# Performance work log

Measured on AMD Instinct MI355X. Metric: run time of the kernel, lower is better.

The kernel has to match this reference:

```python
import jax, jax.numpy as jnp
import numpy as np

B, L, D = 16, 1024, 768

def setup_inputs() -> dict:
    key = jax.random.key(0)
    ks = jax.random.split(key, 6)
    s = 1.0 / np.sqrt(D)  # torch Linear default init scale
    return {
        "h": jax.random.normal(ks[0], (B, L, D), dtype=jnp.float32),
        "q": jax.random.normal(ks[1], (B, L, D), dtype=jnp.float32),
        "w1_w": jax.random.uniform(ks[2], (L, D), jnp.float32, -s, s),
        "w1_b": jax.random.uniform(ks[3], (L,), jnp.float32, -s, s),
        "w2_w": jax.random.uniform(ks[4], (L, D), jnp.float32, -s, s),
        "w2_b": jax.random.uniform(ks[5], (L,), jnp.float32, -s, s),
    }

def reference(h, q, w1_w, w1_b, w2_w, w2_b):
    # w1h: [B, L, l], w2q: [B, L, l] -> permuted [B, l, L]
    w1h = jnp.einsum('bsd,ld->bsl', h, w1_w) + w1_b
    w2q = jnp.einsum('btd,ld->btl', q, w2_w) + w2_b
    w3hq = jnp.einsum('bsd,btd->bst', h, q)           # [B, L, L]
    a = w1h + jnp.swapaxes(w2q, 1, 2) + w3hq          # [B, L, L]
    p = jax.nn.softmax(a, axis=2)
    c = jnp.einsum('bst,btd->bsd', p, q)              # [B, L, D]
    m = jnp.max(a, axis=2)                            # [B, L]
    p2 = jax.nn.softmax(m, axis=1)                    # [B, L]
    qc = h * p2[:, :, None]                           # [B, L, D]
    return jnp.concatenate([h, c, h * c, qc * c], axis=2)  # [B, L, 4D]
```

## Files before the change

kernel.cpp:

```cpp
#include <hip/hip_runtime.h>
#include <stdint.h>

#define B_  16
#define L_  1024
#define D_  768
#define K1_ 1536

typedef unsigned short u16;
typedef __attribute__((ext_vector_type(4))) float f32x4;
typedef __attribute__((ext_vector_type(8))) _Float16 f16x8;

__device__ __forceinline__ u16 f2h(float x){
    return __builtin_bit_cast(u16, (_Float16)x);
}
__device__ __forceinline__ float h2f(u16 x){
    return (float)__builtin_bit_cast(_Float16, x);
}

__device__ __forceinline__ void gload_lds16(const void* g, void* l){
    __builtin_amdgcn_global_load_lds((const __attribute__((address_space(1))) void*)g,
                                     (__attribute__((address_space(3))) void*)l, 16, 0, 0);
}

__global__ __launch_bounds__(256) void prep(const float* __restrict__ h, const float* __restrict__ q,
    const float* __restrict__ w1w, const float* __restrict__ w2w,
    u16* __restrict__ hH, u16* __restrict__ wH, u16* __restrict__ qH,
    u16* __restrict__ w1h, u16* __restrict__ qT, int b0, int nb)
{
    __shared__ float tile[32][33];
    int bb = blockIdx.z, bg = b0 + bb;
    int t0 = blockIdx.x * 32, d0 = blockIdx.y * 32;
    int tid = threadIdx.x;
    int r  = tid >> 3;
    int c4 = (tid & 7) * 4;
    int t = t0 + r, d = d0 + c4;
    size_t goff = (size_t)t * D_ + d;

    float4 qv  = *(const float4*)(q   + (size_t)bg * L_ * D_ + goff);
    float4 hv  = *(const float4*)(h   + (size_t)bg * L_ * D_ + goff);
    float4 w2v = *(const float4*)(w2w + goff);

    tile[r][c4 + 0] = qv.x; tile[r][c4 + 1] = qv.y;
    tile[r][c4 + 2] = qv.z; tile[r][c4 + 3] = qv.w;

    size_t o = ((size_t)bb * L_ + t) * D_ + d;
    ushort4 a;
    a.x = f2h(hv.x); a.y = f2h(hv.y); a.z = f2h(hv.z); a.w = f2h(hv.w);
    *(ushort4*)(hH + o) = a;
    a.x = f2h(hv.x + w2v.x); a.y = f2h(hv.y + w2v.y);
    a.z = f2h(hv.z + w2v.z); a.w = f2h(hv.w + w2v.w);
    *(ushort4*)(wH + o) = a;
    a.x = f2h(qv.x); a.y = f2h(qv.y); a.z = f2h(qv.z); a.w = f2h(qv.w);
    *(ushort4*)(qH + o) = a;
    if (bb == 0){
        float4 w1v = *(const float4*)(w1w + goff);
        a.x = f2h(w1v.x); a.y = f2h(w1v.y); a.z = f2h(w1v.z); a.w = f2h(w1v.w);
        *(ushort4*)(w1h + goff) = a;
    }
    __syncthreads();
    int dr = tid >> 3;
    int tc = (tid & 7) * 4;
    ushort4 b;
    b.x = f2h(tile[tc + 0][dr]); b.y = f2h(tile[tc + 1][dr]);
    b.z = f2h(tile[tc + 2][dr]); b.w = f2h(tile[tc + 3][dr]);
    *(ushort4*)(qT + (size_t)bb * D_ * L_ + (size_t)(d0 + dr) * L_ + t0 + tc) = b;
}

__global__ __launch_bounds__(512) void gemm1(
    const u16* __restrict__ hH, const u16* __restrict__ wH,
    const u16* __restrict__ qH, const u16* __restrict__ w1h,
    const float* __restrict__ w1b, const float* __restrict__ w2b,
    u16* __restrict__ pT, float* __restrict__ mT, float* __restrict__ sT)
{
    __shared__ u16 ldsA[2][256 * 64];
    __shared__ u16 ldsB[2][256 * 64];
    int nwg = gridDim.x;
    int o = blockIdx.x;
    int wg = (o & 7) * (nwg >> 3) + (o >> 3);
    int bb = wg >> 4;
    int tl = wg & 15;
    int smb = tl >> 2, tnb = tl & 3;
    int s0 = smb * 256, t0 = tnb * 256;
    int tid = threadIdx.x;
    int lane = tid & 63, wid = tid >> 6;
    int wm2 = wid >> 2, wn2 = wid & 3;
    int l15 = lane & 15, l4 = lane >> 4;

    const u16* hHb = hH + (size_t)bb * L_ * D_;
    const u16* wHb = wH + (size_t)bb * L_ * D_;
    const u16* qHb = qH + (size_t)bb * L_ * D_;

    f32x4 acc[8][4];
    #pragma unroll
    for (int m = 0; m < 8; m++)
        #pragma unroll
        for (int n = 0; n < 4; n++)
            acc[m][n] = (f32x4){0.f, 0.f, 0.f, 0.f};

    auto stage = [&](int t){
        int kb = t * 64;
        bool inH = (kb < D_);
        const u16* As = inH ? hHb : wHb;
        const u16* Bs = inH ? w1h : qHb;
        int koff = inH ? kb : (kb - D_);
        int buf = t & 1;
        #pragma unroll
        for (int q = 0; q < 4; q++){
            int idx = q * 512 + tid;
            int row = idx >> 3, c = idx & 7;
            int cc = c ^ (row & 7);
            int dst = (q * 512 + wid * 64) * 8;
            gload_lds16(As + (size_t)(s0 + row) * D_ + koff + cc * 8, &ldsA[buf][dst]);
            gload_lds16(Bs + (size_t)(t0 + row) * D_ + koff + cc * 8, &ldsB[buf][dst]);
        }
    };

    stage(0);
    asm volatile("s_waitcnt vmcnt(0)" ::: "memory");
    __builtin_amdgcn_s_barrier();

    for (int t = 0; t < 24; t++){
        if (t + 1 < 24) stage(t + 1);
        int bsel = t & 1;
        #pragma unroll
        for (int kk = 0; kk < 2; kk++){
            f16x8 bf[4];
            #pragma unroll
            for (int n = 0; n < 4; n++){
                int row = wn2 * 64 + n * 16 + l15;
                int c = kk * 4 + l4;
                bf[n] = *(const f16x8*)&ldsB[bsel][(row * 8 + (c ^ (row & 7))) * 8];
            }
            #pragma unroll
            for (int mh = 0; mh < 2; mh++){
                f16x8 af[4];
                #pragma unroll
                for (int mi = 0; mi < 4; mi++){
                    int row = wm2 * 128 + (mh * 4 + mi) * 16 + l15;
                    int c = kk * 4 + l4;
                    af[mi] = *(const f16x8*)&ldsA[bsel][(row * 8 + (c ^ (row & 7))) * 8];
                }
                __builtin_amdgcn_s_setprio(1);
                #pragma unroll
                for (int mi = 0; mi < 4; mi++)
                    #pragma unroll
                    for (int n = 0; n < 4; n++)
                        acc[mh * 4 + mi][n] = __builtin_amdgcn_mfma_f32_16x16x32_f16(
                            af[mi], bf[n], acc[mh * 4 + mi][n], 0, 0, 0);
                __builtin_amdgcn_s_setprio(0);
            }
        }
        asm volatile("s_waitcnt vmcnt(0)" ::: "memory");
        __builtin_amdgcn_s_barrier();
    }

    u16* pRow = pT + (size_t)bb * L_ * L_;
    #pragma unroll
    for (int m = 0; m < 8; m++){
        #pragma unroll
        for (int r = 0; r < 4; r++){
            int s = s0 + wm2 * 128 + m * 16 + l4 * 4 + r;
            float w2v = w2b[s];
            float v[4];
            float tmax = -1e30f;
            #pragma unroll
            for (int n = 0; n < 4; n++){
                int tcol = t0 + wn2 * 64 + n * 16 + l15;
                v[n] = acc[m][n][r] + w1b[tcol] + w2v;
                tmax = fmaxf(tmax, v[n]);
            }
            #pragma unroll
            for (int o2 = 1; o2 < 16; o2 <<= 1)
                tmax = fmaxf(tmax, __shfl_xor(tmax, o2));
            float e[4];
            float gsum = 0.f;
            #pragma unroll
            for (int n = 0; n < 4; n++){
                e[n] = __expf(v[n] - tmax);
                gsum += e[n];
            }
            #pragma unroll
            for (int n = 0; n < 4; n++){
                int tcol = t0 + wn2 * 64 + n * 16 + l15;
                pRow[(size_t)s * L_ + tcol] = f2h(e[n]);
            }
            #pragma unroll
            for (int o2 = 1; o2 < 16; o2 <<= 1)
                gsum += __shfl_xor(gsum, o2);
            if (l15 == 0){
                size_t mo = ((size_t)bb * L_ + s) * 16 + tnb * 4 + wn2;
                mT[mo] = tmax;
                sT[mo] = gsum;
            }
        }
    }
}

__global__ __launch_bounds__(1024) void p2k(const float* __restrict__ mT, const float* __restrict__ sT,
                                            float* __restrict__ p2, float* __restrict__ sc, int b0)
{
    __shared__ float red[16];
    int bb = blockIdx.x, bg = b0 + bb;
    int tid = threadIdx.x;
    const float4* mv = (const float4*)(mT + ((size_t)bb * L_ + tid) * 16);
    float4 m0 = mv[0], m1 = mv[1], m2 = mv[2], m3 = mv[3];
    float mj[16] = {m0.x, m0.y, m0.z, m0.w, m1.x, m1.y, m1.z, m1.w,
                    m2.x, m2.y, m2.z, m2.w, m3.x, m3.y, m3.z, m3.w};
    float v = mj[0];
    #pragma unroll
    for (int i = 1; i < 16; i++) v = fmaxf(v, mj[i]);

    float mx = v;
    #pragma unroll
    for (int o = 32; o; o >>= 1) mx = fmaxf(mx, __shfl_xor(mx, o));
    if ((tid & 63) == 0) red[tid >> 6] = mx;
    __syncthreads();
    float m2g = red[0];
    #pragma unroll
    for (int i = 1; i < 16; i++) m2g = fmaxf(m2g, red[i]);
    float e = __expf(v - m2g);
    float sum = e;
    #pragma unroll
    for (int o = 32; o; o >>= 1) sum += __shfl_xor(sum, o);
    __syncthreads();
    if ((tid & 63) == 0) red[tid >> 6] = sum;
    __syncthreads();
    float st = 0.f;
    #pragma unroll
    for (int i = 0; i < 16; i++) st += red[i];
    p2[(size_t)bg * L_ + tid] = e / st;

    const float4* sv = (const float4*)(sT + ((size_t)bb * L_ + tid) * 16);
    float4 s0v = sv[0], s1v = sv[1], s2v = sv[2], s3v = sv[3];
    float sj[16] = {s0v.x, s0v.y, s0v.z, s0v.w, s1v.x, s1v.y, s1v.z, s1v.w,
                    s2v.x, s2v.y, s2v.z, s2v.w, s3v.x, s3v.y, s3v.z, s3v.w};
    float ej[16];
    float S = 0.f;
    #pragma unroll
    for (int j = 0; j < 16; j++){
        ej[j] = __expf(mj[j] - v);
        S += sj[j] * ej[j];
    }
    float invS = 1.0f / S;
    float* scb = sc + (size_t)bb * 16 * L_;
    #pragma unroll
    for (int j = 0; j < 16; j++)
        scb[j * L_ + tid] = ej[j] * invS;
}

__global__ __launch_bounds__(512) void gemm2(const u16* __restrict__ pT, const u16* __restrict__ qT,
    const float* __restrict__ sc, float* __restrict__ out, int b0)
{
    __shared__ u16 ldsA[2][256 * 64];
    __shared__ u16 ldsB[2][192 * 64];
    int nwg = gridDim.x;
    int o = blockIdx.x;
    int wg = ((nwg & 7) == 0) ? ((o & 7) * (nwg >> 3) + (o >> 3)) : o;
    int bb = wg >> 4;
    int tl = wg & 15;
    int smb = tl >> 2, dnb = tl & 3;
    int s0 = smb * 256, d0 = dnb * 192;
    int tid = threadIdx.x;
    int lane = tid & 63, wid = tid >> 6;
    int wm2 = wid >> 2, wn2 = wid & 3;
    int l15 = lane & 15, l4 = lane >> 4;

    const u16* Ab = pT + (size_t)bb * L_ * L_;
    const u16* Bb = qT + (size_t)bb * D_ * L_;
    const float* scb = sc + (size_t)bb * 16 * L_;

    f32x4 acc[8][3];
    #pragma unroll
    for (int m = 0; m < 8; m++)
        #pragma unroll
        for (int n = 0; n < 3; n++)
            acc[m][n] = (f32x4){0.f, 0.f, 0.f, 0.f};

    auto stage = [&](int t){
        int kb = t * 64;
        int buf = t & 1;
        #pragma unroll
        for (int qq = 0; qq < 4; qq++){
            int idx = qq * 512 + tid;
            int row = idx >> 3, c = idx & 7;
            int cc = c ^ (row & 7);
            gload_lds16(Ab + (size_t)(s0 + row) * L_ + kb + cc * 8,
                        &ldsA[buf][(qq * 512 + wid * 64) * 8]);
        }
        #pragma unroll
        for (int qq = 0; qq < 3; qq++){
            int idx = qq * 512 + tid;
            int row = idx >> 3, c = idx & 7;
            int cc = c ^ (row & 7);
            gload_lds16(Bb + (size_t)(d0 + row) * L_ + kb + cc * 8,
                        &ldsB[buf][(qq * 512 + wid * 64) * 8]);
        }
    };

    stage(0);
    asm volatile("s_waitcnt vmcnt(0)" ::: "memory");
    __builtin_amdgcn_s_barrier();

    for (int t = 0; t < 16; t++){
        if (t + 1 < 16) stage(t + 1);
        int bsel = t & 1;
        _Float16 sch[8];
        #pragma unroll
        for (int m = 0; m < 8; m++)
            sch[m] = (_Float16)scb[(size_t)t * L_ + s0 + wm2 * 128 + m * 16 + l15];
        #pragma unroll
        for (int kk = 0; kk < 2; kk++){
            f16x8 bf[3];
            #pragma unroll
            for (int n = 0; n < 3; n++){
                int row = wn2 * 48 + n * 16 + l15;
                int c = kk * 4 + l4;
                bf[n] = *(const f16x8*)&ldsB[bsel][(row * 8 + (c ^ (row & 7))) * 8];
            }
            #pragma unroll
            for (int mh = 0; mh < 2; mh++){
                f16x8 af[4];
                #pragma unroll
                for (int mi = 0; mi < 4; mi++){
                    int row = wm2 * 128 + (mh * 4 + mi) * 16 + l15;
                    int c = kk * 4 + l4;
                    af[mi] = *(const f16x8*)&ldsA[bsel][(row * 8 + (c ^ (row & 7))) * 8];
                    af[mi] = af[mi] * sch[mh * 4 + mi];
                }
                __builtin_amdgcn_s_setprio(1);
                #pragma unroll
                for (int mi = 0; mi < 4; mi++)
                    #pragma unroll
                    for (int n = 0; n < 3; n++)
                        acc[mh * 4 + mi][n] = __builtin_amdgcn_mfma_f32_16x16x32_f16(
                            af[mi], bf[n], acc[mh * 4 + mi][n], 0, 0, 0);
                __builtin_amdgcn_s_setprio(0);
            }
        }
        asm volatile("s_waitcnt vmcnt(0)" ::: "memory");
        __builtin_amdgcn_s_barrier();
    }

    float* oC = out + ((size_t)(b0 + bb) * L_) * (4 * D_) + D_;
    #pragma unroll
    for (int m = 0; m < 8; m++){
        int sbase = s0 + wm2 * 128 + m * 16 + l4 * 4;
        #pragma unroll
        for (int r = 0; r < 4; r++){
            int s = sbase + r;
            #pragma unroll
            for (int n = 0; n < 3; n++){
                int d = d0 + wn2 * 48 + n * 16 + l15;
                oC[(size_t)s * (4 * D_) + d] = acc[m][n][r];
            }
        }
    }
}

__global__ __launch_bounds__(192) void epi(const u16* __restrict__ hH,
    const float* __restrict__ p2, float* __restrict__ out, int b0)
{
    int rowid = blockIdx.x;
    int bb = rowid >> 10, s = rowid & 1023;
    int bg = b0 + bb;
    float p2v = p2[(size_t)bg * L_ + s];
    const u16* hR = hH + ((size_t)bb * L_ + s) * D_;
    float* oR = out + ((size_t)bg * L_ + s) * (4 * D_);
    int d = threadIdx.x * 4;
    float4 cv = *(const float4*)(oR + D_ + d);
    ushort4 hu = *(const ushort4*)(hR + d);
    float4 hv = {h2f(hu.x), h2f(hu.y), h2f(hu.z), h2f(hu.w)};
    float4 hc = {hv.x * cv.x, hv.y * cv.y, hv.z * cv.z, hv.w * cv.w};
    float4 qc = {p2v * hc.x, p2v * hc.y, p2v * hc.z, p2v * hc.w};
    *(float4*)(oR + d)          = hv;
    *(float4*)(oR + 2 * D_ + d) = hc;
    *(float4*)(oR + 3 * D_ + d) = qc;
}

extern "C" void kernel_launch(void* const* d_in, const int* in_sizes, int n_in,
                              void* d_out, int out_size, void* d_ws, size_t ws_size,
                              hipStream_t stream)
{
    const float* h   = (const float*)d_in[0];
    const float* q   = (const float*)d_in[1];
    const float* w1w = (const float*)d_in[2];
    const float* w1b = (const float*)d_in[3];
    const float* w2w = (const float*)d_in[4];
    const float* w2b = (const float*)d_in[5];
    float* out = (float*)d_out;

    const size_t szPlane = (size_t)L_ * D_ * 2;
    const size_t szM     = (size_t)B_ * L_ * 4;
    const size_t perB_pT = (size_t)L_ * L_ * 2;
    const size_t perB_s  = (size_t)L_ * 16 * 4;
    const size_t perB = 4 * szPlane + perB_pT + 3 * perB_s;
    const size_t fixed = szPlane + szM;

    int NB = 1;
    if (ws_size > fixed){
        size_t nbc = (ws_size - fixed) / perB;
        NB = (nbc >= 16) ? 16 : (nbc < 1 ? 1 : (int)nbc);
    }

    char* p = (char*)d_ws;
    u16*   w1h  = (u16*)p;   p += szPlane;
    float* p2   = (float*)p; p += szM;
    float* mT   = (float*)p; p += perB_s * NB;
    float* sT   = (float*)p; p += perB_s * NB;
    float* sc   = (float*)p; p += perB_s * NB;
    u16*   hH   = (u16*)p;   p += szPlane * NB;
    u16*   wH   = (u16*)p;   p += szPlane * NB;
    u16*   qH   = (u16*)p;   p += szPlane * NB;
    u16*   qT   = (u16*)p;   p += szPlane * NB;
    u16*   pT   = (u16*)p;

    for (int b0 = 0; b0 < B_; b0 += NB){
        int nb = (B_ - b0 < NB) ? (B_ - b0) : NB;
        prep  <<<dim3(32, 24, nb), 256, 0, stream>>>(h, q, w1w, w2w, hH, wH, qH, w1h, qT, b0, nb);
        gemm1 <<<dim3(16 * nb), 512, 0, stream>>>(hH, wH, qH, w1h, w1b, w2b, pT, mT, sT);
        p2k   <<<dim3(nb), 1024, 0, stream>>>(mT, sT, p2, sc, b0);
        gemm2 <<<dim3(16 * nb), 512, 0, stream>>>(pT, qT, sc, out, b0);
        epi   <<<dim3(nb * 1024), 192, 0, stream>>>(hH, p2, out, b0);
    }
}
```

Measured before the change: 193.9 us.

## Factor score GEMM as (h+w2)(w1+q) minus precomputed w2·w1 to halve K

The fused score GEMM used to concatenate two K=768 products ([h, h+w2]·[w1, q]). It now computes one K=768 product of (h+w2) and (w1+q), then subtracts a batch-independent w2·w1 term. That term is computed once by a new small GEMM kernel into an fp32 workspace and read back in the softmax epilogue. This halves the MFMA work and the operand loads in the main GEMM. In exchange it adds a one-time 16-block GEMM, extra fp32 reads of C0 per tile, more workspace, and possible fp16 rounding and cancellation error from the summed operands.

```diff
diff --git a/kernel.cpp b/kernel.cpp
--- a/kernel.cpp
+++ b/kernel.cpp
@@ -4,7 +4,6 @@
 #define B_  16
 #define L_  1024
 #define D_  768
-#define K1_ 1536
 
 typedef unsigned short u16;
 typedef __attribute__((ext_vector_type(4))) float f32x4;
@@ -24,8 +23,8 @@
 
 __global__ __launch_bounds__(256) void prep(const float* __restrict__ h, const float* __restrict__ q,
     const float* __restrict__ w1w, const float* __restrict__ w2w,
-    u16* __restrict__ hH, u16* __restrict__ wH, u16* __restrict__ qH,
-    u16* __restrict__ w1h, u16* __restrict__ qT, int b0, int nb)
+    u16* __restrict__ hH, u16* __restrict__ wH, u16* __restrict__ B1,
+    u16* __restrict__ w1h, u16* __restrict__ w2h, u16* __restrict__ qT, int b0, int nb)
 {
     __shared__ float tile[32][33];
     int bb = blockIdx.z, bg = b0 + bb;
@@ -39,6 +38,7 @@
     float4 qv  = *(const float4*)(q   + (size_t)bg * L_ * D_ + goff);
     float4 hv  = *(const float4*)(h   + (size_t)bg * L_ * D_ + goff);
     float4 w2v = *(const float4*)(w2w + goff);
+    float4 w1v = *(const float4*)(w1w + goff);
 
     tile[r][c4 + 0] = qv.x; tile[r][c4 + 1] = qv.y;
     tile[r][c4 + 2] = qv.z; tile[r][c4 + 3] = qv.w;
@@ -50,12 +50,14 @@
     a.x = f2h(hv.x + w2v.x); a.y = f2h(hv.y + w2v.y);
     a.z = f2h(hv.z + w2v.z); a.w = f2h(hv.w + w2v.w);
     *(ushort4*)(wH + o) = a;
-    a.x = f2h(qv.x); a.y = f2h(qv.y); a.z = f2h(qv.z); a.w = f2h(qv.w);
-    *(ushort4*)(qH + o) = a;
+    a.x = f2h(w1v.x + qv.x); a.y = f2h(w1v.y + qv.y);
+    a.z = f2h(w1v.z + qv.z); a.w = f2h(w1v.w + qv.w);
+    *(ushort4*)(B1 + o) = a;
     if (bb == 0){
-        float4 w1v = *(const float4*)(w1w + goff);
         a.x = f2h(w1v.x); a.y = f2h(w1v.y); a.z = f2h(w1v.z); a.w = f2h(w1v.w);
         *(ushort4*)(w1h + goff) = a;
+        a.x = f2h(w2v.x); a.y = f2h(w2v.y); a.z = f2h(w2v.z); a.w = f2h(w2v.w);
+        *(ushort4*)(w2h + goff) = a;
     }
     __syncthreads();
     int dr = tid >> 3;
@@ -66,10 +68,96 @@
     *(ushort4*)(qT + (size_t)bb * D_ * L_ + (size_t)(d0 + dr) * L_ + t0 + tc) = b;
 }
 
+__global__ __launch_bounds__(512) void c0k(const u16* __restrict__ w2h, const u16* __restrict__ w1h,
+                                           float* __restrict__ C0)
+{
+    __shared__ u16 ldsA[2][256 * 64];
+    __shared__ u16 ldsB[2][256 * 64];
+    int tl = blockIdx.x;
+    int smb = tl >> 2, tnb = tl & 3;
+    int s0 = smb * 256, t0 = tnb * 256;
+    int tid = threadIdx.x;
+    int lane = tid & 63, wid = tid >> 6;
+    int wm2 = wid >> 2, wn2 = wid & 3;
+    int l15 = lane & 15, l4 = lane >> 4;
+
+    f32x4 acc[8][4];
+    #pragma unroll
+    for (int m = 0; m < 8; m++)
+        #pragma unroll
+        for (int n = 0; n < 4; n++)
+            acc[m][n] = (f32x4){0.f, 0.f, 0.f, 0.f};
+
+    auto stage = [&](int t){
+        int kb = t * 64;
+        int buf = t & 1;
+        #pragma unroll
+        for (int q = 0; q < 4; q++){
+            int idx = q * 512 + tid;
+            int row = idx >> 3, c = idx & 7;
+            int cc = c ^ (row & 7);
+            int dst = (q * 512 + wid * 64) * 8;
+            gload_lds16(w2h + (size_t)(s0 + row) * D_ + kb + cc * 8, &ldsA[buf][dst]);
+            gload_lds16(w1h + (size_t)(t0 + row) * D_ + kb + cc * 8, &ldsB[buf][dst]);
+        }
+    };
+
+    stage(0);
+    asm volatile("s_waitcnt vmcnt(0)" ::: "memory");
+    __builtin_amdgcn_s_barrier();
+
+    for (int t = 0; t < 12; t++){
+        if (t + 1 < 12) stage(t + 1);
+        int bsel = t & 1;
+        #pragma unroll
+        for (int kk = 0; kk < 2; kk++){
+            f16x8 bf[4];
+            #pragma unroll
+            for (int n = 0; n < 4; n++){
+                int row = wn2 * 64 + n * 16 + l15;
+                int c = kk * 4 + l4;
+                bf[n] = *(const f16x8*)&ldsB[bsel][(row * 8 + (c ^ (row & 7))) * 8];
+            }
+            #pragma unroll
+            for (int mh = 0; mh < 2; mh++){
+                f16x8 af[4];
+                #pragma unroll
+                for (int mi = 0; mi < 4; mi++){
+                    int row = wm2 * 128 + (mh * 4 + mi) * 16 + l15;
+                    int c = kk * 4 + l4;
+                    af[mi] = *(const f16x8*)&ldsA[bsel][(row * 8 + (c ^ (row & 7))) * 8];
+                }
+                #pragma unroll
+                for (int mi = 0; mi < 4; mi++)
+                    #pragma unroll
+                    for (int n = 0; n < 4; n++)
+                        acc[mh * 4 + mi][n] = __builtin_amdgcn_mfma_f32_16x16x32_f16(
+                            af[mi], bf[n], acc[mh * 4 + mi][n], 0, 0, 0);
+            }
+        }
+        asm volatile("s_waitcnt vmcnt(0)" ::: "memory");
+        __builtin_amdgcn_s_barrier();
+    }
+
+    #pragma unroll
+    for (int m = 0; m < 8; m++){
+        int sbase = s0 + wm2 * 128 + m * 16 + l4 * 4;
+        #pragma unroll
+        for (int r = 0; r < 4; r++){
+            int s = sbase + r;
+            #pragma unroll
+            for (int n = 0; n < 4; n++){
+                int tcol = t0 + wn2 * 64 + n * 16 + l15;
+                C0[(size_t)s * L_ + tcol] = acc[m][n][r];
+            }
+        }
+    }
+}
+
 __global__ __launch_bounds__(512) void gemm1(
-    const u16* __restrict__ hH, const u16* __restrict__ wH,
-    const u16* __restrict__ qH, const u16* __restrict__ w1h,
+    const u16* __restrict__ wH, const u16* __restrict__ B1,
     const float* __restrict__ w1b, const float* __restrict__ w2b,
+    const float* __restrict__ C0,
     u16* __restrict__ pT, float* __restrict__ mT, float* __restrict__ sT)
 {
     __shared__ u16 ldsA[2][256 * 64];
@@ -86,9 +174,8 @@
     int wm2 = wid >> 2, wn2 = wid & 3;
     int l15 = lane & 15, l4 = lane >> 4;
 
-    const u16* hHb = hH + (size_t)bb * L_ * D_;
-    const u16* wHb = wH + (size_t)bb * L_ * D_;
-    const u16* qHb = qH + (size_t)bb * L_ * D_;
+    const u16* Ab = wH + (size_t)bb * L_ * D_;
+    const u16* Bb = B1 + (size_t)bb * L_ * D_;
 
     f32x4 acc[8][4];
     #pragma unroll
@@ -99,10 +186,6 @@
 
     auto stage = [&](int t){
         int kb = t * 64;
-        bool inH = (kb < D_);
-        const u16* As = inH ? hHb : wHb;
-        const u16* Bs = inH ? w1h : qHb;
-        int koff = inH ? kb : (kb - D_);
         int buf = t & 1;
         #pragma unroll
         for (int q = 0; q < 4; q++){
@@ -110,8 +193,8 @@
             int row = idx >> 3, c = idx & 7;
             int cc = c ^ (row & 7);
             int dst = (q * 512 + wid * 64) * 8;
-            gload_lds16(As + (size_t)(s0 + row) * D_ + koff + cc * 8, &ldsA[buf][dst]);
-            gload_lds16(Bs + (size_t)(t0 + row) * D_ + koff + cc * 8, &ldsB[buf][dst]);
+            gload_lds16(Ab + (size_t)(s0 + row) * D_ + kb + cc * 8, &ldsA[buf][dst]);
+            gload_lds16(Bb + (size_t)(t0 + row) * D_ + kb + cc * 8, &ldsB[buf][dst]);
         }
     };
 
@@ -119,8 +202,8 @@
     asm volatile("s_waitcnt vmcnt(0)" ::: "memory");
     __builtin_amdgcn_s_barrier();
 
-    for (int t = 0; t < 24; t++){
-        if (t + 1 < 24) stage(t + 1);
+    for (int t = 0; t < 12; t++){
+        if (t + 1 < 12) stage(t + 1);
         int bsel = t & 1;
         #pragma unroll
         for (int kk = 0; kk < 2; kk++){
@@ -161,12 +244,13 @@
         for (int r = 0; r < 4; r++){
             int s = s0 + wm2 * 128 + m * 16 + l4 * 4 + r;
             float w2v = w2b[s];
+            const float* c0r = C0 + (size_t)s * L_;
             float v[4];
             float tmax = -1e30f;
             #pragma unroll
             for (int n = 0; n < 4; n++){
                 int tcol = t0 + wn2 * 64 + n * 16 + l15;
-                v[n] = acc[m][n][r] + w1b[tcol] + w2v;
+                v[n] = acc[m][n][r] - c0r[tcol] + w1b[tcol] + w2v;
                 tmax = fmaxf(tmax, v[n]);
             }
             #pragma unroll
@@ -391,10 +475,11 @@
 
     const size_t szPlane = (size_t)L_ * D_ * 2;
     const size_t szM     = (size_t)B_ * L_ * 4;
+    const size_t szC0    = (size_t)L_ * L_ * 4;
     const size_t perB_pT = (size_t)L_ * L_ * 2;
     const size_t perB_s  = (size_t)L_ * 16 * 4;
     const size_t perB = 4 * szPlane + perB_pT + 3 * perB_s;
-    const size_t fixed = szPlane + szM;
+    const size_t fixed = 2 * szPlane + szC0 + szM;
 
     int NB = 1;
     if (ws_size > fixed){
@@ -404,20 +489,24 @@
 
     char* p = (char*)d_ws;
     u16*   w1h  = (u16*)p;   p += szPlane;
+    u16*   w2h  = (u16*)p;   p += szPlane;
+    float* C0   = (float*)p; p += szC0;
     float* p2   = (float*)p; p += szM;
     float* mT   = (float*)p; p += perB_s * NB;
     float* sT   = (float*)p; p += perB_s * NB;
     float* sc   = (float*)p; p += perB_s * NB;
     u16*   hH   = (u16*)p;   p += szPlane * NB;
     u16*   wH   = (u16*)p;   p += szPlane * NB;
-    u16*   qH   = (u16*)p;   p += szPlane * NB;
+    u16*   B1   = (u16*)p;   p += szPlane * NB;
     u16*   qT   = (u16*)p;   p += szPlane * NB;
     u16*   pT   = (u16*)p;
 
     for (int b0 = 0; b0 < B_; b0 += NB){
         int nb = (B_ - b0 < NB) ? (B_ - b0) : NB;
-        prep  <<<dim3(32, 24, nb), 256, 0, stream>>>(h, q, w1w, w2w, hH, wH, qH, w1h, qT, b0, nb);
-        gemm1 <<<dim3(16 * nb), 512, 0, stream>>>(hH, wH, qH, w1h, w1b, w2b, pT, mT, sT);
+        prep  <<<dim3(32, 24, nb), 256, 0, stream>>>(h, q, w1w, w2w, hH, wH, B1, w1h, w2h, qT, b0, nb);
+        if (b0 == 0)
+            c0k <<<dim3(16), 512, 0, stream>>>(w2h, w1h, C0);
+        gemm1 <<<dim3(16 * nb), 512, 0, stream>>>(wH, B1, w1b, w2b, C0, pT, mT, sT);
         p2k   <<<dim3(nb), 1024, 0, stream>>>(mT, sT, p2, sc, b0);
         gemm2 <<<dim3(16 * nb), 512, 0, stream>>>(pT, qT, sc, out, b0);
         epi   <<<dim3(nb * 1024), 192, 0, stream>>>(hH, p2, out, b0);
```

New measurement: 209.4 us. 8.0% more time.
